# Kernel optimization log

Hardware: AMD Instinct MI355X
Metric: run time of the kernel (lower is better)

Reference implementation:

```python
import jax, jax.numpy as jnp
import numpy as np

EPS = 1e-4
SILU_GAIN = 1.0 / 0.596  # magnitude-preserving SiLU gain
SCALES = (4, 4, 8)       # prod == A_DIM == 128
T = 0.3                  # residual lerp weight


def mp_silu(x):
    return jax.nn.silu(x) * SILU_GAIN


def pixel_norm(x):
    # normalize over channel dim (axis=1) to unit RMS
    return x * jax.lax.rsqrt(jnp.mean(jnp.square(x), axis=1, keepdims=True) + EPS)


def norm_w(w):
    # magnitude-preserving conv: per-output-filter L2-normalized weight
    n = jnp.sqrt(jnp.sum(jnp.square(w), axis=tuple(range(1, w.ndim)), keepdims=True) + 1e-8)
    return w / n


def mp_add(a, b, t=T):
    return (a * (1.0 - t) + b * t) / np.sqrt((1.0 - t) ** 2 + t ** 2)


def conv2d(x, w, groups=1, padding=((0, 0), (0, 0))):
    return jax.lax.conv_general_dilated(
        x, w, (1, 1), padding,
        dimension_numbers=('NCHW', 'OIHW', 'NCHW'), feature_group_count=groups)


def conv1d(x, w, groups=1, padding=((0, 0),)):
    return jax.lax.conv_general_dilated(
        x, w, (1,), padding,
        dimension_numbers=('NCH', 'OIH', 'NCH'), feature_group_count=groups)


def avgpool_freq(x, s):
    B, C, F, L = x.shape
    return jnp.mean(x.reshape(B, C, F // s, s, L), axis=3)


def min_gru(h, w):
    # minGRU: z_t = sigmoid(Wz h_t), c_t = Wc h_t, s_t = (1-z_t) s_{t-1} + z_t c_t
    z, c = jnp.split(conv1d(h, norm_w(w)), 2, axis=1)
    z = jax.nn.sigmoid(z)
    a, b = 1.0 - z, z * c  # linear recurrence s_t = a_t s_{t-1} + b_t

    def comb(x, y):
        a1, b1 = x
        a2, b2 = y
        return a2 * a1, a2 * b1 + b2

    _, out = jax.lax.associative_scan(comb, (a, b), axis=-1)
    return out


def conv_block(x, w1, wd, w2, wdn, s):
    # x: [B, d, F, L]
    x = pixel_norm(x)
    r = mp_silu(x)
    r = conv2d(r, norm_w(w1))                                            # d -> h, 1x1
    r = conv2d(r, norm_w(wd), groups=wd.shape[0], padding=((2, 2), (1, 1)))  # depthwise 5x3
    r = mp_silu(r)
    r = conv2d(r, norm_w(w2))                                            # h -> d, 1x1
    h = mp_add(x, r)
    return conv2d(avgpool_freq(h, s), norm_w(wdn))                       # d -> 2d, freq /s


def seq_block(x, hg_w, dw_w, gru_w, out_w):
    # x: [B, d, L]
    x = pixel_norm(x)
    h, g = jnp.split(conv1d(x, norm_w(hg_w)), 2, axis=1)  # each [B, H, L]
    h = mp_silu(h)
    h = conv1d(h, norm_w(dw_w), groups=dw_w.shape[0], padding=((1, 1),))  # depthwise k=3
    h = mp_silu(h)
    h = min_gru(h, gru_w)
    h = h * mp_silu(g)
    return mp_add(x, conv1d(h, norm_w(out_w)))


def setup_inputs() -> dict:
    key = jax.random.key(0)
    ks = jax.random.split(key, 18)
    rn = lambda k, s: jax.random.normal(k, s, dtype=jnp.float32)
    B, L, A = 2, 2048, 128
    return {
        'audio': rn(ks[0], (B, A, L)),
        'proj_w': rn(ks[1], (64, 1, 1, 1)) * 0.5,
        'proj_b': jnp.zeros((64,), jnp.float32),
        'c0_w1': rn(ks[2], (128, 64, 1, 1)),
        'c0_wd': rn(ks[3], (128, 1, 5, 3)),
        'c0_w2': rn(ks[4], (64, 128, 1, 1)),
        'c0_dn': rn(ks[5], (128, 64, 1, 1)),
        'c1_w1': rn(ks[6], (256, 128, 1, 1)),
        'c1_wd': rn(ks[7], (256, 1, 5, 3)),
        'c1_w2': rn(ks[8], (128, 256, 1, 1)),
        'c1_dn': rn(ks[9], (256, 128, 1, 1)),
        'c2_w1': rn(ks[10], (512, 256, 1, 1)),
        'c2_wd': rn(ks[11], (512, 1, 5, 3)),
        'c2_w2': rn(ks[12], (256, 512, 1, 1)),
        'c2_dn': rn(ks[13], (512, 256, 1, 1)),
        'hg_w': rn(ks[14], (4, 2048, 512, 1)),
        'dw_w': rn(ks[15], (4, 1024, 1, 3)),
        'gru_w': rn(ks[16], (4, 2048, 1024, 1)),
        'out_w': rn(ks[17], (4, 512, 1024, 1)),
    }


def reference(audio, proj_w, proj_b,
              c0_w1, c0_wd, c0_w2, c0_dn,
              c1_w1, c1_wd, c1_w2, c1_dn,
              c2_w1, c2_wd, c2_w2, c2_dn,
              hg_w, dw_w, gru_w, out_w):
    h = audio[:, None]  # [B, 1, A_DIM, L]
    h = conv2d(h, proj_w) + proj_b[None, :, None, None]
    blocks = ((c0_w1, c0_wd, c0_w2, c0_dn),
              (c1_w1, c1_wd, c1_w2, c1_dn),
              (c2_w1, c2_wd, c2_w2, c2_dn))
    for (w1, wd, w2, dn), s in zip(blocks, SCALES):
        h = conv_block(h, w1, wd, w2, dn, s)
    h = h[:, :, 0, :]  # freq dim reduced to 1 -> [B, dim, L]
    for i in range(hg_w.shape[0]):
        h = seq_block(h, hg_w[i], dw_w[i], gru_w[i], out_w[i])
    return mp_silu(h)
```

## Files before the change

### kernel.cpp

```cpp
#include <hip/hip_runtime.h>
#include <math.h>

#define GAIN 1.6778523489932886f
#define MPS  1.3130643285972254f

typedef __attribute__((ext_vector_type(8))) short short8;
typedef __attribute__((ext_vector_type(4))) short short4v;
typedef __attribute__((ext_vector_type(4))) float float4v;

__device__ __forceinline__ float silu_g(float x){
  float s = 1.0f/(1.0f + __expf(-x));
  return x*s*GAIN;
}
__device__ __forceinline__ short f2bf(float f){
  unsigned u = __builtin_bit_cast(unsigned, f);
  u += 0x7fffu + ((u >> 16) & 1u);
  return (short)(u >> 16);
}
__device__ __forceinline__ float bf2f(unsigned short h){
  return __builtin_bit_cast(float, ((unsigned)h) << 16);
}

typedef __attribute__((address_space(3))) unsigned int as3_uint;
typedef const __attribute__((address_space(1))) unsigned int as1_cuint;
__device__ __forceinline__ void gload16(const unsigned short* gsrc, unsigned short* ldst){
  __builtin_amdgcn_global_load_lds((as1_cuint*)gsrc, (as3_uint*)ldst, 16, 0, 0);
}

struct NcEnt { const float* w; int O, K, dstOff; };
struct NcArgs { NcEnt e[16]; };

__global__ __launch_bounds__(64) void normcast_kernel(NcArgs na, unsigned short* __restrict__ wbf){
  int row = blockIdx.x;
  int base = 0; int i;
  for (i = 0; i < 16; i++){
    if (row < base + na.e[i].O) break;
    base += na.e[i].O;
  }
  if (i >= 16) return;
  int r = row - base; int K = na.e[i].K;
  const float* w = na.e[i].w + (long)r*K;
  unsigned short* dst = wbf + na.e[i].dstOff + (long)r*K;
  int tid = threadIdx.x;
  float s = 0.f;
  const bool v4 = ((K & 3) == 0);
  if (v4){
    for (int k = tid*4; k < K; k += 256){
      float4v v = *(const float4v*)&w[k];
      s += v[0]*v[0] + v[1]*v[1] + v[2]*v[2] + v[3]*v[3];
    }
  } else {
    for (int k = tid; k < K; k += 64){ float v = w[k]; s += v*v; }
  }
  for (int off = 32; off; off >>= 1) s += __shfl_down(s, off);
  float inv = rsqrtf(__shfl(s, 0) + 1e-8f);
  if (v4){
    for (int k = tid*4; k < K; k += 256){
      float4v v = *(const float4v*)&w[k];
      short4v o = { f2bf(v[0]*inv), f2bf(v[1]*inv), f2bf(v[2]*inv), f2bf(v[3]*inv) };
      *(short4v*)&dst[k] = o;
    }
  } else {
    for (int k = tid; k < K; k += 64) dst[k] = (unsigned short)f2bf(w[k]*inv);
  }
}

__global__ __launch_bounds__(64) void projstats_kernel(const float* __restrict__ pw, const float* __restrict__ pb,
                                                       float* __restrict__ S){
  int t = threadIdx.x;
  float p = pw[t], q = pb[t];
  float s1 = p*p, s2 = p*q, s3 = q*q;
  for (int off = 32; off; off >>= 1){
    s1 += __shfl_down(s1, off); s2 += __shfl_down(s2, off); s3 += __shfl_down(s3, off);
  }
  if (t == 0){ S[0] = s1; S[1] = s2; S[2] = s3; }
}

__global__ __launch_bounds__(256) void invn_audio_kernel(const float* __restrict__ audio, const float* __restrict__ S,
                                                         float* __restrict__ invn){
  long i = blockIdx.x*256 + threadIdx.x;
  if (i >= (2L*128*2048)/4) return;
  long e = i*4;
  float S1 = S[0], S2 = S[1], S3 = S[2];
  float4v a = *(const float4v*)&audio[e];
  float4v o;
  #pragma unroll
  for (int j = 0; j < 4; j++) o[j] = rsqrtf((a[j]*a[j]*S1 + 2.f*a[j]*S2 + S3)/64.f + 1e-4f);
  *(float4v*)&invn[e] = o;
}

template<int G, bool BF>
__global__ __launch_bounds__(256) void invn_reduce_kernel(const void* __restrict__ Xv, float* __restrict__ invn,
                                                          int C, int F){
  constexpr int L = 256/G;
  int t = threadIdx.x; int cs = t / L; int li = t % L;
  long pos = (long)blockIdx.x*L + li;
  int bf = (int)(pos >> 11); int l = (int)(pos & 2047);
  int b = bf / F; int f = bf - b*F;
  long base = ((long)b*C*F + f)*2048 + l;
  long stride = (long)F*2048;
  float s = 0.f;
  if (BF){
    const unsigned short* X = (const unsigned short*)Xv;
    for (int c = cs; c < C; c += G){ float v = bf2f(X[base + (long)c*stride]); s += v*v; }
  } else {
    const float* X = (const float*)Xv;
    for (int c = cs; c < C; c += G){ float v = X[base + (long)c*stride]; s += v*v; }
  }
  __shared__ float red[256];
  red[t] = s; __syncthreads();
  #pragma unroll
  for (int off = G/2; off > 0; off >>= 1){
    if (cs < off) red[t] += red[t + off*L];
    __syncthreads();
  }
  if (cs == 0) invn[pos] = rsqrtf(red[li]/(float)C + 1e-4f);
}

__global__ __launch_bounds__(256) void normT_kernel(const float* __restrict__ SEQ,
                                                    const float* __restrict__ invn,
                                                    unsigned short* __restrict__ XST){
  __shared__ float tile[64][65];
  const int l0 = blockIdx.x*64, c0 = blockIdx.y*64, b = blockIdx.z;
  const int t = threadIdx.x;
  const int lr = (t & 15)*4;
  const int cr = t >> 4;
  #pragma unroll
  for (int p = 0; p < 4; p++){
    int c = cr + p*16;
    float4v v = *(const float4v*)&SEQ[((long)(b*512 + c0 + c))*2048 + l0 + lr];
    tile[c][lr+0] = v[0]; tile[c][lr+1] = v[1]; tile[c][lr+2] = v[2]; tile[c][lr+3] = v[3];
  }
  __syncthreads();
  const int cc = (t & 7)*8;
  const int lw = t >> 3;
  #pragma unroll
  for (int p = 0; p < 2; p++){
    int l = lw + p*32;
    float iv = invn[b*2048 + l0 + l];
    short8 o;
    #pragma unroll
    for (int j = 0; j < 8; j++) o[j] = f2bf(tile[cc+j][l] * iv);
    *(short8*)&XST[((long)(b*2048 + l0 + l))*512 + c0 + cc] = o;
  }
}

struct GTArgs {
  const unsigned short* A;
  const unsigned short* B;
  unsigned short* O1;
  unsigned short* O2;
  int N, K;
};

template<int EMODE>
__global__ __launch_bounds__(256,2) void gemmT_kernel(GTArgs g){
  __shared__ __align__(16) char SMEMraw[49152];
  unsigned short (*Asm)[4096] = (unsigned short (*)[4096])SMEMraw;
  unsigned short (*Bsm)[4096] = (unsigned short (*)[4096])(SMEMraw + 24576);
  const int t = threadIdx.x;
  const int lane = t & 63;
  const int wc = (t >> 7) & 1;
  const int wsd = (t >> 6) & 1;
  const int q = lane >> 4, r16 = lane & 15;
  const int m0 = blockIdx.x * 128;
  const int n0 = blockIdx.y * 128;
  const int K = g.K;

  const int r0 = t >> 2;
  const int c8 = (((t & 3) ^ ((r0 >> 1) & 3)) << 3);
  const unsigned short* Ap = g.A + (long)(n0 + r0)*K + c8;
  const unsigned short* Bp = g.B + (long)(m0 + r0)*K + c8;

  auto stage = [&](int bi, int k0){
    gload16(Ap + k0,           &Asm[bi][t*8]);
    gload16(Ap + 64*K + k0,    &Asm[bi][2048 + t*8]);
    gload16(Bp + k0,           &Bsm[bi][t*8]);
    gload16(Bp + 64*K + k0,    &Bsm[bi][2048 + t*8]);
  };

  float4v acc[4][4];
  #pragma unroll
  for (int i = 0; i < 4; i++)
    #pragma unroll
    for (int j = 0; j < 4; j++) acc[i][j] = (float4v){0.f,0.f,0.f,0.f};

  const int nit = K >> 5;
  stage(0, 0);
  stage(1, 32);

  const int qsw = ((q ^ ((r16 >> 1) & 3)) << 3);

  for (int it = 0; it < nit; ++it){
    if (it + 2 < nit){
      stage((it + 2) % 3, (it + 2) << 5);
      asm volatile("" ::: "memory");
      asm volatile("s_waitcnt vmcnt(8)" ::: "memory");
    } else if (it + 1 < nit){
      asm volatile("s_waitcnt vmcnt(4)" ::: "memory");
    } else {
      asm volatile("s_waitcnt vmcnt(0)" ::: "memory");
    }
    __builtin_amdgcn_s_barrier();
    asm volatile("" ::: "memory");

    const unsigned short* As = Asm[it % 3];
    const unsigned short* Bs = Bsm[it % 3];
    short8 afr[4], bfr[4];
    #pragma unroll
    for (int i = 0; i < 4; i++) afr[i] = *(const short8*)&As[(wc*64 + i*16 + r16)*32 + qsw];
    #pragma unroll
    for (int j = 0; j < 4; j++) bfr[j] = *(const short8*)&Bs[(wsd*64 + j*16 + r16)*32 + qsw];
    #pragma unroll
    for (int i = 0; i < 4; i++)
      #pragma unroll
      for (int j = 0; j < 4; j++)
        acc[i][j] = __builtin_amdgcn_mfma_f32_16x16x32_bf16(afr[i], bfr[j], acc[i][j], 0, 0, 0);

    asm volatile("" ::: "memory");
    __builtin_amdgcn_s_barrier();
  }

  if (EMODE == 1 && n0 < 1024){
    float* Cf = (float*)SMEMraw;
    #pragma unroll
    for (int h = 0; h < 2; h++){
      __syncthreads();
      if (wc == h){
        #pragma unroll
        for (int j = 0; j < 4; j++){
          int m = wsd*64 + j*16 + r16;
          #pragma unroll
          for (int i = 0; i < 4; i++)
            *(float4v*)&Cf[m*68 + i*16 + q*4] = acc[i][j];
        }
      }
      __syncthreads();
      #pragma unroll
      for (int p = 0; p < 4; p++){
        int m = (t >> 3) + p*32;
        int n8 = (t & 7)*8;
        int gm = m0 + m; int b = gm >> 11, l = gm & 2047;
        float4v v0 = *(const float4v*)&Cf[m*68 + n8];
        float4v v1 = *(const float4v*)&Cf[m*68 + n8 + 4];
        short8 o;
        #pragma unroll
        for (int e = 0; e < 4; e++){ o[e] = f2bf(silu_g(v0[e])); o[e+4] = f2bf(silu_g(v1[e])); }
        *(short8*)&g.O1[((long)(b*2048 + l))*1024 + (n0 + h*64 + n8)] = o;
      }
    }
  } else {
    float* Csm = (float*)SMEMraw;
    #pragma unroll
    for (int qtr = 0; qtr < 4; qtr++){
      __syncthreads();
      if (wc == (qtr >> 1)){
        #pragma unroll
        for (int ii = 0; ii < 2; ii++){
          int i = (qtr & 1)*2 + ii;
          #pragma unroll
          for (int j = 0; j < 4; j++){
            int m = wsd*64 + j*16 + r16;
            #pragma unroll
            for (int rg = 0; rg < 4; rg++)
              Csm[(ii*16 + q*4 + rg)*132 + m] = acc[i][j][rg];
          }
        }
      }
      __syncthreads();
      #pragma unroll
      for (int sp = 0; sp < 2; sp++){
        int nrow = (t >> 4) + sp*16;
        int n = n0 + qtr*32 + nrow;
        int m8 = (t & 15)*8;
        int gm = m0 + m8; int b = gm >> 11, l = gm & 2047;
        float4v v0 = *(const float4v*)&Csm[nrow*132 + m8];
        float4v v1 = *(const float4v*)&Csm[nrow*132 + m8 + 4];
        short8 o;
        #pragma unroll
        for (int e = 0; e < 4; e++){ o[e] = f2bf(v0[e]); o[e+4] = f2bf(v1[e]); }
        if (EMODE == 1) *(short8*)&g.O2[((long)(b*1024 + (n - 1024)))*2048 + l] = o;
        else            *(short8*)&g.O1[((long)(b*2048 + n))*2048 + l] = o;
      }
    }
  }
}

struct GemmArgs {
  const unsigned short* A;
  const unsigned short* Bh;
  const float* invn; const float* audio;
  const float* pw; const float* pb;
  const unsigned short* auxXH;
  unsigned short* CoutH; unsigned short* Cout2H;
  int N, K, Fdim, Lw, lq0, BLw, Bl0, CLw, Cl0, Nsto, Fsrc;
};

template<int BMODE, int EMODE>
__global__ __launch_bounds__(256,2) void mgemm_kernel(GemmArgs g){
  __shared__ __align__(16) char SMEMraw[20480];
  unsigned short* Asm = (unsigned short*)SMEMraw;
  unsigned short* Bsm = Asm + 128*40;
  const int t = threadIdx.x;
  const int lane = t & 63;
  const int wave = t >> 6;
  const int wc = wave >> 1, wsd = wave & 1;
  const int q = lane >> 4, r16 = lane & 15;
  const int s0 = blockIdx.x * 128;
  const int n0 = blockIdx.y * 128;
  const int FL = g.Fdim * g.Lw;

  const int ar = t >> 1, ah = t & 1;
  const int an = n0 + ar;
  const bool aval = an < g.N;
  const unsigned short* Aptr = g.A + (long)an*g.K + ah*16;

  const int kg = t & 7, mg = t >> 3;
  const int mb = s0 + mg*4;
  int bcol = mb / FL; int rr = mb - bcol*FL;
  int fcol = (g.Fdim > 1) ? (rr / g.Lw) : 0;
  int labs = g.lq0 + (rr - fcol*g.Lw);
  const bool cv = (bcol < 2);
  bool lv[4];
  #pragma unroll
  for (int j = 0; j < 4; j++) lv[j] = cv && (labs + j >= 0) && (labs + j < 2048);
  const bool vec4 = cv && (labs >= 0) && (labs + 3 < 2048);
  const unsigned short* bbase = g.Bh;
  if (cv) bbase = g.Bh + ((long)(bcol*g.K)*g.Fsrc + fcol)*g.BLw + (labs - g.Bl0);
  const long kstep = (long)g.Fsrc * g.BLw;

  float invn4[4] = {0,0,0,0}, aud4[4] = {0,0,0,0};
  if (BMODE == 2 || BMODE == 3){
    #pragma unroll
    for (int j = 0; j < 4; j++) if (lv[j]){
      invn4[j] = g.invn[(bcol*g.Fdim + fcol)*2048 + labs + j];
      if (BMODE == 2) aud4[j] = g.audio[(bcol*128 + fcol)*2048 + labs + j];
    }
  }

  float4v acc[4][4];
  #pragma unroll
  for (int i = 0; i < 4; i++)
    #pragma unroll
    for (int j = 0; j < 4; j++) acc[i][j] = (float4v){0.f,0.f,0.f,0.f};

  short8 pa0 = {0,0,0,0,0,0,0,0}, pa1 = {0,0,0,0,0,0,0,0};
  short4v praw[4];
  #pragma unroll
  for (int i = 0; i < 4; i++) praw[i] = (short4v){0,0,0,0};

  auto ldA = [&](int kb){
    if (aval){
      pa0 = *(const short8*)(Aptr + kb);
      pa1 = *(const short8*)(Aptr + kb + 8);
    }
  };
  auto ldB = [&](int kb){
    #pragma unroll
    for (int i = 0; i < 4; i++){
      const int k = kb + kg*4 + i;
      const unsigned short* bp = bbase + (long)k*kstep;
      if (vec4) praw[i] = *(const short4v*)bp;
      else {
        short4v u = {0,0,0,0};
        #pragma unroll
        for (int j = 0; j < 4; j++) if (lv[j]) u[j] = (short)bp[j];
        praw[i] = u;
      }
    }
  };

  ldA(0);
  if (BMODE != 2) ldB(0);

  for (int k0 = 0; k0 < g.K; k0 += 32){
    short8 sa0 = pa0, sa1 = pa1;
    short4v bpk[4];
    if (BMODE == 0){
      #pragma unroll
      for (int j = 0; j < 4; j++){
        short4v p;
        #pragma unroll
        for (int i = 0; i < 4; i++) p[i] = praw[i][j];
        bpk[j] = p;
      }
    } else if (BMODE == 3){
      #pragma unroll
      for (int j = 0; j < 4; j++){
        short4v p;
        #pragma unroll
        for (int i = 0; i < 4; i++)
          p[i] = f2bf(silu_g(bf2f((unsigned short)praw[i][j]) * invn4[j]));
        bpk[j] = p;
      }
    } else {
      float tv[4][4];
      #pragma unroll
      for (int i = 0; i < 4; i++){
        const int k = k0 + kg*4 + i;
        const float pwk = g.pw[k], pbk = g.pb[k];
        #pragma unroll
        for (int j = 0; j < 4; j++) tv[i][j] = lv[j] ? silu_g((aud4[j]*pwk + pbk)*invn4[j]) : 0.f;
      }
      #pragma unroll
      for (int j = 0; j < 4; j++){
        short4v p;
        #pragma unroll
        for (int i = 0; i < 4; i++) p[i] = f2bf(tv[i][j]);
        bpk[j] = p;
      }
    }
    if (k0 + 32 < g.K){
      ldA(k0 + 32);
      if (BMODE != 2) ldB(k0 + 32);
    }

    __syncthreads();
    *(short8*)&Asm[ar*40 + ah*16]     = sa0;
    *(short8*)&Asm[ar*40 + ah*16 + 8] = sa1;
    #pragma unroll
    for (int j = 0; j < 4; j++)
      *(short4v*)&Bsm[(mg*4 + j)*40 + kg*4] = bpk[j];
    __syncthreads();

    short8 afr[4], bfr[4];
    #pragma unroll
    for (int i = 0; i < 4; i++) afr[i] = *(const short8*)&Asm[(wc*64 + i*16 + r16)*40 + q*8];
    #pragma unroll
    for (int j = 0; j < 4; j++) bfr[j] = *(const short8*)&Bsm[(wsd*64 + j*16 + r16)*40 + q*8];
    #pragma unroll
    for (int i = 0; i < 4; i++)
      #pragma unroll
      for (int j = 0; j < 4; j++)
        acc[i][j] = __builtin_amdgcn_mfma_f32_16x16x32_bf16(afr[i], bfr[j], acc[i][j], 0, 0, 0);
  }

  {
    float* Csm = (float*)SMEMraw;
    #pragma unroll
    for (int qtr = 0; qtr < 4; qtr++){
      __syncthreads();
      if (wc == (qtr >> 1)){
        #pragma unroll
        for (int ii = 0; ii < 2; ii++){
          int i = (qtr & 1)*2 + ii;
          #pragma unroll
          for (int j = 0; j < 4; j++){
            int m = wsd*64 + j*16 + r16;
            #pragma unroll
            for (int rg = 0; rg < 4; rg++)
              Csm[(ii*16 + q*4 + rg)*132 + m] = acc[i][j][rg];
          }
        }
      }
      __syncthreads();
      #pragma unroll
      for (int sp = 0; sp < 2; sp++){
        int nrow = (t >> 4) + sp*16;
        int n = n0 + qtr*32 + nrow;
        int m8 = (t & 15)*8;
        if (n >= g.N) continue;
        int sg = s0 + m8;
        int b2 = sg / FL; int r2 = sg - b2*FL;
        if (b2 >= 2) continue;
        int f2 = (g.Fdim > 1) ? (r2 / g.Lw) : 0;
        int l2 = g.lq0 + (r2 - f2*g.Lw);
        float4v v0 = *(const float4v*)&Csm[nrow*132 + m8];
        float4v v1 = *(const float4v*)&Csm[nrow*132 + m8 + 4];
        long obase = ((long)(b2*g.Nsto + n)*g.Fdim + f2)*g.CLw + (l2 - g.Cl0);
        short8 o;
        if (EMODE == 1){
          #pragma unroll
          for (int e = 0; e < 4; e++){ o[e] = f2bf(v0[e]); o[e+4] = f2bf(v1[e]); }
        } else if (EMODE == 2){
          short8 axv = *(const short8*)&g.auxXH[((long)(b2*g.N + n)*g.Fdim + f2)*2048 + l2];
          const float* ivp = &g.invn[(b2*g.Fdim + f2)*2048 + l2];
          float4v iv0 = *(const float4v*)ivp;
          float4v iv1 = *(const float4v*)(ivp + 4);
          #pragma unroll
          for (int e = 0; e < 4; e++){
            float xn0 = bf2f((unsigned short)axv[e]) * iv0[e];
            float xn1 = bf2f((unsigned short)axv[e+4]) * iv1[e];
            o[e]   = f2bf((xn0*0.7f + v0[e]*0.3f)*MPS);
            o[e+4] = f2bf((xn1*0.7f + v1[e]*0.3f)*MPS);
          }
        } else {
          float pwn = g.pw[n], pbn = g.pb[n];
          const float* ap  = &g.audio[(b2*128 + f2)*2048 + l2];
          const float* ivp = &g.invn[(b2*g.Fdim + f2)*2048 + l2];
          float4v a0 = *(const float4v*)ap,  a1 = *(const float4v*)(ap + 4);
          float4v iv0 = *(const float4v*)ivp, iv1 = *(const float4v*)(ivp + 4);
          #pragma unroll
          for (int e = 0; e < 4; e++){
            float xn0 = (a0[e]*pwn + pbn)*iv0[e];
            float xn1 = (a1[e]*pwn + pbn)*iv1[e];
            o[e]   = f2bf((xn0*0.7f + v0[e]*0.3f)*MPS);
            o[e+4] = f2bf((xn1*0.7f + v1[e]*0.3f)*MPS);
          }
        }
        *(short8*)&g.CoutH[obase] = o;
      }
    }
  }
}

struct DnArgs {
  const unsigned short* A; const unsigned short* P;
  float* Cout; unsigned short* CoutH;
  int N, K, F2, Lc, l0;
};

template<int EMODE>
__global__ __launch_bounds__(256,4) void mgemm64_kernel(DnArgs g){
  __shared__ __align__(16) char SMEM[10240];
  unsigned short* Asm = (unsigned short*)SMEM;
  unsigned short* Bsm = Asm + 64*40;
  const int t = threadIdx.x;
  const int lane = t & 63;
  const int wave = t >> 6;
  const int wc = wave >> 1, wsd = wave & 1;
  const int q = lane >> 4, r16 = lane & 15;
  const int s0 = blockIdx.x * 64;
  const int n0 = blockIdx.y * 64;
  const int FL = g.F2 * g.Lc;

  const int ar = t >> 2, ah = t & 3;
  const unsigned short* Aptr = g.A + (long)(n0 + ar)*g.K + ah*8;
  const int kg = t & 7, mg = t >> 3;
  const bool bstage = (mg < 16);
  const int mb = s0 + (mg & 15)*4;
  const int bcol = mb / FL; const int rr = mb - bcol*FL;
  const int fcol = rr / g.Lc; const int li = rr - fcol*g.Lc;
  const unsigned short* bbase = g.P + ((long)(bcol*g.K)*g.F2 + fcol)*g.Lc + li;
  const long kstep = (long)g.F2 * g.Lc;

  float4v acc[2][2];
  #pragma unroll
  for (int i = 0; i < 2; i++)
    #pragma unroll
    for (int j = 0; j < 2; j++) acc[i][j] = (float4v){0.f,0.f,0.f,0.f};

  short8 pa = {0,0,0,0,0,0,0,0};
  short4v praw[4];
  #pragma unroll
  for (int i = 0; i < 4; i++) praw[i] = (short4v){0,0,0,0};

  auto ldA = [&](int kb){ pa = *(const short8*)(Aptr + kb); };
  auto ldB = [&](int kb){
    if (bstage){
      #pragma unroll
      for (int i = 0; i < 4; i++)
        praw[i] = *(const short4v*)(bbase + (long)(kb + kg*4 + i)*kstep);
    }
  };
  ldA(0); ldB(0);

  for (int k0 = 0; k0 < g.K; k0 += 32){
    short8 sa = pa;
    short4v bpk[4];
    #pragma unroll
    for (int j = 0; j < 4; j++){
      short4v p;
      #pragma unroll
      for (int i = 0; i < 4; i++) p[i] = praw[i][j];
      bpk[j] = p;
    }
    if (k0 + 32 < g.K){ ldA(k0 + 32); ldB(k0 + 32); }

    __syncthreads();
    *(short8*)&Asm[ar*40 + ah*8] = sa;
    if (bstage){
      #pragma unroll
      for (int j = 0; j < 4; j++)
        *(short4v*)&Bsm[((mg & 15)*4 + j)*40 + kg*4] = bpk[j];
    }
    __syncthreads();

    short8 afr[2], bfr[2];
    #pragma unroll
    for (int i = 0; i < 2; i++) afr[i] = *(const short8*)&Asm[(wc*32 + i*16 + r16)*40 + q*8];
    #pragma unroll
    for (int j = 0; j < 2; j++) bfr[j] = *(const short8*)&Bsm[(wsd*32 + j*16 + r16)*40 + q*8];
    #pragma unroll
    for (int i = 0; i < 2; i++)
      #pragma unroll
      for (int j = 0; j < 2; j++)
        acc[i][j] = __builtin_amdgcn_mfma_f32_16x16x32_bf16(afr[i], bfr[j], acc[i][j], 0, 0, 0);
  }

  {
    float* Csm = (float*)SMEM;
    const int b2 = s0 / FL; const int r20 = s0 - b2*FL;
    const int f2c = r20 / g.Lc; const int l2c = g.l0 + (r20 - f2c*g.Lc);
    #pragma unroll
    for (int nq = 0; nq < 4; nq++){
      __syncthreads();
      if (wc == (nq >> 1)){
        const int i = nq & 1;
        #pragma unroll
        for (int j = 0; j < 2; j++)
          #pragma unroll
          for (int rg = 0; rg < 4; rg++)
            Csm[(q*4 + rg)*68 + wsd*32 + j*16 + r16] = acc[i][j][rg];
      }
      __syncthreads();
      int nrow = t >> 4;
      int mq = (t & 15)*4;
      int n = n0 + nq*16 + nrow;
      float4v v = *(const float4v*)&Csm[nrow*68 + mq];
      long oidx = ((long)(b2*g.N + n)*g.F2 + f2c)*2048 + l2c + mq;
      if (EMODE == 0){
        *(float4v*)&g.Cout[oidx] = v;
      } else {
        short4v o = { f2bf(v[0]), f2bf(v[1]), f2bf(v[2]), f2bf(v[3]) };
        *(short4v*)&g.CoutH[oidx] = o;
      }
    }
  }
}

template<int EMODE>
__global__ __launch_bounds__(256,4) void seqout_kernel(const unsigned short* __restrict__ A,
                                                       const unsigned short* __restrict__ Bh,
                                                       const float* __restrict__ invn,
                                                       const float* __restrict__ auxX,
                                                       float* __restrict__ Cout, int K){
  __shared__ __align__(16) char SMEM[10240];
  unsigned short* Asm = (unsigned short*)SMEM;
  unsigned short* Bsm = Asm + 64*40;
  const int t = threadIdx.x;
  const int lane = t & 63;
  const int wave = t >> 6;
  const int wc = wave >> 1, wsd = wave & 1;
  const int q = lane >> 4, r16 = lane & 15;
  const int s0 = blockIdx.x * 64;
  const int n0 = blockIdx.y * 64;

  const int ar = t >> 2, ah = t & 3;
  const unsigned short* Aptr = A + (long)(n0 + ar)*K + ah*8;
  const int kg = t & 7, mg = t >> 3;
  const bool bstage = (mg < 16);
  const int mb = s0 + (mg & 15)*4;
  const int bcol = mb >> 11, lb = mb & 2047;
  const unsigned short* bbase = Bh + ((long)bcol*K)*2048 + lb;

  float4v acc[2][2];
  #pragma unroll
  for (int i = 0; i < 2; i++)
    #pragma unroll
    for (int j = 0; j < 2; j++) acc[i][j] = (float4v){0.f,0.f,0.f,0.f};

  short8 pa = {0,0,0,0,0,0,0,0};
  short4v praw[4];
  #pragma unroll
  for (int i = 0; i < 4; i++) praw[i] = (short4v){0,0,0,0};

  auto ldA = [&](int kb){ pa = *(const short8*)(Aptr + kb); };
  auto ldB = [&](int kb){
    if (bstage){
      #pragma unroll
      for (int i = 0; i < 4; i++)
        praw[i] = *(const short4v*)(bbase + (long)(kb + kg*4 + i)*2048);
    }
  };
  ldA(0); ldB(0);

  for (int k0 = 0; k0 < K; k0 += 32){
    short8 sa = pa;
    short4v bpk[4];
    #pragma unroll
    for (int j = 0; j < 4; j++){
      short4v p;
      #pragma unroll
      for (int i = 0; i < 4; i++) p[i] = praw[i][j];
      bpk[j] = p;
    }
    if (k0 + 32 < K){ ldA(k0 + 32); ldB(k0 + 32); }

    __syncthreads();
    *(short8*)&Asm[ar*40 + ah*8] = sa;
    if (bstage){
      #pragma unroll
      for (int j = 0; j < 4; j++)
        *(short4v*)&Bsm[((mg & 15)*4 + j)*40 + kg*4] = bpk[j];
    }
    __syncthreads();

    short8 afr[2], bfr[2];
    #pragma unroll
    for (int i = 0; i < 2; i++) afr[i] = *(const short8*)&Asm[(wc*32 + i*16 + r16)*40 + q*8];
    #pragma unroll
    for (int j = 0; j < 2; j++) bfr[j] = *(const short8*)&Bsm[(wsd*32 + j*16 + r16)*40 + q*8];
    #pragma unroll
    for (int i = 0; i < 2; i++)
      #pragma unroll
      for (int j = 0; j < 2; j++)
        acc[i][j] = __builtin_amdgcn_mfma_f32_16x16x32_bf16(afr[i], bfr[j], acc[i][j], 0, 0, 0);
  }

  {
    float* Csm = (float*)SMEM;
    const int b2 = s0 >> 11; const int l0b = s0 & 2047;
    #pragma unroll
    for (int nq = 0; nq < 4; nq++){
      __syncthreads();
      if (wc == (nq >> 1)){
        const int i = nq & 1;
        #pragma unroll
        for (int j = 0; j < 2; j++)
          #pragma unroll
          for (int rg = 0; rg < 4; rg++)
            Csm[(q*4 + rg)*68 + wsd*32 + j*16 + r16] = acc[i][j][rg];
      }
      __syncthreads();
      int nrow = t >> 4;
      int mq = (t & 15)*4;
      int n = n0 + nq*16 + nrow;
      int l = l0b + mq;
      float4v v = *(const float4v*)&Csm[nrow*68 + mq];
      float4v ax = *(const float4v*)&auxX[((long)b2*512 + n)*2048 + l];
      float4v iv = *(const float4v*)&invn[b2*2048 + l];
      float4v r;
      #pragma unroll
      for (int e = 0; e < 4; e++){
        float xn = ax[e]*iv[e];
        float rr = (xn*0.7f + v[e]*0.3f)*MPS;
        r[e] = (EMODE == 6) ? silu_g(rr) : rr;
      }
      *(float4v*)&Cout[((long)b2*512 + n)*2048 + l] = r;
    }
  }
}

__global__ __launch_bounds__(256) void poolf_kernel(const unsigned short* __restrict__ Hb,
                                                    unsigned short* __restrict__ P,
                                                    int F2, int s, int Lc, long total4){
  long i = blockIdx.x*256 + threadIdx.x;
  if (i >= total4) return;
  long e = i*4;
  int li = (int)(e % Lc); long r0 = e / Lc;
  int f2 = (int)(r0 % F2); long r = r0 / F2;
  const unsigned short* src = Hb + ((long)r*F2*s + (long)f2*s)*Lc + li;
  float a0=0,a1=0,a2=0,a3=0;
  for (int p = 0; p < s; p++){
    short4v u = *(const short4v*)(src + (long)p*Lc);
    a0 += bf2f((unsigned short)u[0]); a1 += bf2f((unsigned short)u[1]);
    a2 += bf2f((unsigned short)u[2]); a3 += bf2f((unsigned short)u[3]);
  }
  float inv = 1.f/(float)s;
  short4v o = { f2bf(a0*inv), f2bf(a1*inv), f2bf(a2*inv), f2bf(a3*inv) };
  *(short4v*)&P[((long)r*F2 + f2)*Lc + li] = o;
}

struct DwArgs { const unsigned short* R1; const unsigned short* wd; unsigned short* R2; int C, F, Lc, l0; };
__global__ __launch_bounds__(256) void dw2d_kernel(DwArgs a){
  int idx = blockIdx.x*256 + threadIdx.x;
  int Lq = a.Lc >> 3;
  int Fq = a.F >> 2;
  int total = 2*a.C*Fq*Lq;
  if (idx >= total) return;
  int lq = idx % Lq; int r = idx / Lq;
  int fq = r % Fq; r /= Fq;
  int c = r % a.C; int b = r / a.C;
  int f0 = fq*4;
  int labs = a.l0 + lq*8;
  int Lw = a.Lc + 8;
  const unsigned short* base = a.R1 + (long)((b*a.C + c)*a.F)*Lw + (labs - (a.l0 - 4));
  const unsigned short* w = a.wd + c*15;
  float W[5][3];
  #pragma unroll
  for (int tp = 0; tp < 5; tp++)
    #pragma unroll
    for (int j = 0; j < 3; j++) W[tp][j] = bf2f(w[tp*3 + j]);

  const bool llo = (labs > 0);
  const bool lhi = (labs + 8 < 2048);
  float acc[4][8];
  #pragma unroll
  for (int t = 0; t < 4; t++)
    #pragma unroll
    for (int j = 0; j < 8; j++) acc[t][j] = 0.f;

  #pragma unroll
  for (int r8 = 0; r8 < 8; r8++){
    int rrow = f0 - 2 + r8;
    if (rrow < 0 || rrow >= a.F) continue;
    const unsigned short* p = base + (long)rrow*Lw;
    short4v u0 = *(const short4v*)p;
    short4v u1 = *(const short4v*)(p + 4);
    float x[10];
    x[0] = llo ? bf2f(p[-1]) : 0.f;
    x[1] = bf2f((unsigned short)u0[0]); x[2] = bf2f((unsigned short)u0[1]);
    x[3] = bf2f((unsigned short)u0[2]); x[4] = bf2f((unsigned short)u0[3]);
    x[5] = bf2f((unsigned short)u1[0]); x[6] = bf2f((unsigned short)u1[1]);
    x[7] = bf2f((unsigned short)u1[2]); x[8] = bf2f((unsigned short)u1[3]);
    x[9] = lhi ? bf2f(p[8]) : 0.f;
    #pragma unroll
    for (int t = 0; t < 4; t++){
      const int df = r8 - 2 - t;
      if (df < -2 || df > 2) continue;
      float w0 = W[df+2][0], w1 = W[df+2][1], w2 = W[df+2][2];
      #pragma unroll
      for (int j = 0; j < 8; j++)
        acc[t][j] += w0*x[j] + w1*x[j+1] + w2*x[j+2];
    }
  }

  unsigned short* ob = a.R2 + ((long)((b*a.C + c)*a.F + f0))*a.Lc + (labs - a.l0);
  #pragma unroll
  for (int t = 0; t < 4; t++){
    short8 o;
    #pragma unroll
    for (int j = 0; j < 8; j++) o[j] = f2bf(silu_g(acc[t][j]));
    *(short8*)(ob + (long)t*a.Lc) = o;
  }
}

__global__ __launch_bounds__(256) void dwseqT_kernel(const unsigned short* __restrict__ HST,
                                                     const unsigned short* __restrict__ w,
                                                     unsigned short* __restrict__ H2T){
  int idx = blockIdx.x*256 + threadIdx.x;
  if (idx >= 2*2048*128) return;
  int c0 = (idx & 127) * 8; long bt = idx >> 7;
  int tt = (int)(bt & 2047);
  const unsigned short* base = HST + bt*1024 + c0;
  short8 zz = {0,0,0,0,0,0,0,0};
  short8 x1 = *(const short8*)base;
  short8 x0 = (tt > 0)    ? *(const short8*)(base - 1024) : zz;
  short8 x2 = (tt < 2047) ? *(const short8*)(base + 1024) : zz;
  const unsigned short* wp = w + c0*3;
  short8 o;
  #pragma unroll
  for (int j = 0; j < 8; j++){
    float w0 = bf2f(wp[3*j]), w1 = bf2f(wp[3*j+1]), w2 = bf2f(wp[3*j+2]);
    float v = w0*bf2f((unsigned short)x0[j]) + w1*bf2f((unsigned short)x1[j]) + w2*bf2f((unsigned short)x2[j]);
    o[j] = f2bf(silu_g(v));
  }
  *(short8*)&H2T[bt*1024 + c0] = o;
}

__global__ __launch_bounds__(256) void scan_kernel(const unsigned short* __restrict__ ZC, const unsigned short* __restrict__ G,
                                                   unsigned short* __restrict__ SC){
  int bc = blockIdx.x;
  int b = bc >> 10, c = bc & 1023;
  const unsigned short* zrow = ZC + ((long)(b*2048 + c))*2048;
  const unsigned short* crow = ZC + ((long)(b*2048 + 1024 + c))*2048;
  const unsigned short* grow = G + (long)bc*2048;
  unsigned short* orow = SC + (long)bc*2048;
  int tid = threadIdx.x;
  int t0 = tid*8;
  short8 zv = *(const short8*)&zrow[t0];
  short8 cv = *(const short8*)&crow[t0];
  float av[8], bv[8];
  float A = 1.f, Bv = 0.f;
  #pragma unroll
  for (int j = 0; j < 8; j++){
    float z = bf2f((unsigned short)zv[j]); float cval = bf2f((unsigned short)cv[j]);
    float zs = 1.f/(1.f + __expf(-z));
    float a = 1.f - zs; float bb = zs*cval;
    av[j] = a; bv[j] = bb;
    Bv = a*Bv + bb;
    A = a*A;
  }
  __shared__ float sA[256], sB[256];
  sA[tid] = A; sB[tid] = Bv;
  __syncthreads();
  for (int off = 1; off < 256; off <<= 1){
    float pA = 1.f, pB = 0.f;
    if (tid >= off){ pA = sA[tid-off]; pB = sB[tid-off]; }
    __syncthreads();
    float nA = A*pA; float nB = A*pB + Bv;
    A = nA; Bv = nB;
    sA[tid] = A; sB[tid] = Bv;
    __syncthreads();
  }
  float h = (tid > 0) ? sB[tid-1] : 0.f;
  short8 gv = *(const short8*)&grow[t0];
  short8 ov;
  #pragma unroll
  for (int j = 0; j < 8; j++){
    h = av[j]*h + bv[j];
    ov[j] = f2bf(h * silu_g(bf2f((unsigned short)gv[j])));
  }
  *(short8*)&orow[t0] = ov;
}

extern "C" void kernel_launch(void* const* d_in, const int* in_sizes, int n_in,
                              void* d_out, int out_size, void* d_ws, size_t ws_size,
                              hipStream_t stream) {
  const float* audio = (const float*)d_in[0];
  const float* pw = (const float*)d_in[1];
  const float* pb = (const float*)d_in[2];
  const float* cw1[3] = {(const float*)d_in[3], (const float*)d_in[7], (const float*)d_in[11]};
  const float* cwd[3] = {(const float*)d_in[4], (const float*)d_in[8], (const float*)d_in[12]};
  const float* cw2[3] = {(const float*)d_in[5], (const float*)d_in[9], (const float*)d_in[13]};
  const float* cdn[3] = {(const float*)d_in[6], (const float*)d_in[10], (const float*)d_in[14]};
  const float* hgw  = (const float*)d_in[15];
  const float* dww  = (const float*)d_in[16];
  const float* gruw = (const float*)d_in[17];
  const float* outw = (const float*)d_in[18];
  float* out = (float*)d_out;

  char* P0 = (char*)d_ws;
  float*          INVW = (float*)P0;                    P0 += 131072;
  unsigned short* WBF  = (unsigned short*)P0;           P0 += 30443776;
  float*          INVN = (float*)P0;                    P0 += 2097152;
  char*           XBZC = P0;                            P0 += 33554432;
  unsigned short* IN1h = (unsigned short*)P0;           P0 += 33554432;
  unsigned short* IN2h = (unsigned short*)P0;           P0 += 16777216;
  float*          SEQ  = (float*)P0;                    P0 += 8388608;
  char*           ARENA = P0;
  long arenaBytes = (long)ws_size - (long)(P0 - (char*)d_ws);
  float* S = INVW + 32000;

  const float* wsrc[16] = {cw1[0],cwd[0],cw2[0],cdn[0], cw1[1],cwd[1],cw2[1],cdn[1],
                           cw1[2],cwd[2],cw2[2],cdn[2], hgw, dww, gruw, outw};
  int Os[16] = {128,128,64,128, 256,256,128,256, 512,512,256,512, 8192,4096,8192,2048};
  int Ks[16] = {64,15,128,64, 128,15,256,128, 256,15,512,256, 512,3,1024,1024};
  int wbfOff[16];
  {
    int wo = 0;
    for (int i = 0; i < 16; i++){ wbfOff[i] = wo; wo += Os[i]*Ks[i]; }
  }
  {
    NcArgs na;
    int rows = 0;
    for (int i = 0; i < 16; i++){
      na.e[i].w = wsrc[i]; na.e[i].O = Os[i]; na.e[i].K = Ks[i]; na.e[i].dstOff = wbfOff[i];
      rows += Os[i];
    }
    normcast_kernel<<<rows, 64, 0, stream>>>(na, WBF);
  }
  projstats_kernel<<<1, 64, 0, stream>>>(pw, pb, S);

  int Cin_[3]  = {64,128,256};
  int Cmid_[3] = {128,256,512};
  int F_[3]    = {128,32,8};
  int s_[3]    = {4,4,8};
  const unsigned short* XinH[3] = {nullptr, IN1h, IN2h};
  unsigned short* XoutH[3] = {IN1h, IN2h, nullptr};
  int iW1[3]={0,4,8}, iWd[3]={1,5,9}, iW2[3]={2,6,10}, iDn[3]={3,7,11};

  for (int b = 0; b < 3; b++){
    int Cin = Cin_[b], Cmid = Cmid_[b], F = F_[b], s = s_[b];
    int F2 = F/s;
    int nc = 16;
    for (int c = 1; c <= 16; c <<= 1){
      long Lc = 2048/c;
      long bytes = 2L*(2L*Cmid*F*(Lc+8) + 2L*Cmid*F*Lc + 2L*Cin*F*Lc + 2L*Cin*F2*Lc);
      if (bytes <= arenaBytes){ nc = c; break; }
    }
    int Lc = 2048/nc;
    unsigned short* R1 = (unsigned short*)ARENA;
    unsigned short* R2 = R1 + 2L*Cmid*F*(Lc+8);
    unsigned short* Hb = R2 + 2L*Cmid*F*Lc;
    unsigned short* Pb = Hb + 2L*Cin*F*Lc;

    if (b == 0){
      invn_audio_kernel<<<(2*128*2048/4+255)/256, 256, 0, stream>>>(audio, S, INVN);
    } else {
      int positions = 2*F*2048;
      invn_reduce_kernel<8,true><<<positions/32, 256, 0, stream>>>(XinH[b], INVN, Cin, F);
    }

    for (int ci = 0; ci < nc; ci++){
      int l0 = ci*Lc;
      GemmArgs ga{};
      ga.A = WBF + wbfOff[iW1[b]];
      ga.Bh = XinH[b]; ga.invn = INVN; ga.audio = audio; ga.pw = pw; ga.pb = pb;
      ga.CoutH = R1; ga.N = Cmid; ga.K = Cin; ga.Fdim = F; ga.Lw = Lc+8; ga.lq0 = l0-4;
      ga.BLw = 2048; ga.Bl0 = 0; ga.CLw = Lc+8; ga.Cl0 = l0-4; ga.Nsto = Cmid; ga.Fsrc = F;
      int M1 = 2*F*(Lc+8);
      dim3 g1((M1+127)/128, (Cmid+127)/128);
      if (b == 0) mgemm_kernel<2,1><<<g1,256,0,stream>>>(ga);
      else        mgemm_kernel<3,1><<<g1,256,0,stream>>>(ga);
      DwArgs da{R1, WBF + wbfOff[iWd[b]], R2, Cmid, F, Lc, l0};
      int tdw = 2*Cmid*(F/4)*(Lc/8);
      dw2d_kernel<<<(tdw+255)/256, 256, 0, stream>>>(da);
      GemmArgs gb{};
      gb.A = WBF + wbfOff[iW2[b]];
      gb.Bh = R2; gb.invn = INVN; gb.audio = audio; gb.pw = pw; gb.pb = pb; gb.auxXH = XinH[b];
      gb.CoutH = Hb; gb.N = Cin; gb.K = Cmid; gb.Fdim = F; gb.Lw = Lc; gb.lq0 = l0;
      gb.BLw = Lc; gb.Bl0 = l0; gb.CLw = Lc; gb.Cl0 = l0; gb.Nsto = Cin; gb.Fsrc = F;
      int M2 = 2*F*Lc;
      dim3 g2((M2+127)/128, (Cin+127)/128);
      if (b == 0) mgemm_kernel<0,3><<<g2,256,0,stream>>>(gb);
      else        mgemm_kernel<0,2><<<g2,256,0,stream>>>(gb);
      long tp4 = (2L*Cin*F2*Lc)/4;
      poolf_kernel<<<(int)((tp4+255)/256), 256, 0, stream>>>(Hb, Pb, F2, s, Lc, tp4);
      DnArgs dn{};
      dn.A = WBF + wbfOff[iDn[b]]; dn.P = Pb;
      dn.Cout = SEQ; dn.CoutH = XoutH[b];
      dn.N = Cmid; dn.K = Cin; dn.F2 = F2; dn.Lc = Lc; dn.l0 = l0;
      dim3 gdn((2*F2*Lc)/64, Cmid/64);
      if (b == 2) mgemm64_kernel<0><<<gdn,256,0,stream>>>(dn);
      else        mgemm64_kernel<1><<<gdn,256,0,stream>>>(dn);
    }
  }

  unsigned short* XST = IN1h;
  unsigned short* HST = XST + 2097152;
  unsigned short* G   = HST + 4194304;
  unsigned short* H2T = G  + 4194304;
  unsigned short* SC  = H2T + 4194304;
  unsigned short* ZCh = (unsigned short*)XBZC;

  for (int i = 0; i < 4; i++){
    invn_reduce_kernel<16,false><<<4096/16, 256, 0, stream>>>(SEQ, INVN, 512, 1);
    normT_kernel<<<dim3(32,8,2), 256, 0, stream>>>(SEQ, INVN, XST);
    GTArgs gh{ WBF + wbfOff[12] + (long)i*2048*512, XST, HST, G, 2048, 512 };
    gemmT_kernel<1><<<dim3(32,16), 256, 0, stream>>>(gh);
    dwseqT_kernel<<<2048, 256, 0, stream>>>(HST, WBF + wbfOff[13] + i*1024*3, H2T);
    GTArgs gz{ WBF + wbfOff[14] + (long)i*2048*1024, H2T, ZCh, nullptr, 2048, 1024 };
    gemmT_kernel<0><<<dim3(32,16), 256, 0, stream>>>(gz);
    scan_kernel<<<2048,256,0,stream>>>(ZCh, G, SC);
    const unsigned short* oA = WBF + wbfOff[15] + (long)i*512*1024;
    if (i < 3) seqout_kernel<5><<<dim3(64,8),256,0,stream>>>(oA, SC, INVN, SEQ, SEQ, 1024);
    else       seqout_kernel<6><<<dim3(64,8),256,0,stream>>>(oA, SC, INVN, SEQ, out, 1024);
  }

  (void)in_sizes; (void)n_in; (void)out_size;
}
```

Before: 1.108 ms.

## Precompute normalized SiLU input once and widen depthwise conv frequency tile

For conv blocks 1 and 2, a new elementwise kernel applies pixel-norm scaling and SiLU to the block input once, writing a bf16 buffer. The first 1x1 GEMM then reads that buffer as a plain operand instead of recomputing the norm and SiLU inside every GEMM tile. Separately, the depthwise 5x3 kernel now computes 8 frequency rows per thread instead of 4, so more outputs share each loaded row. The trade-off is an extra full read and write of the activation tensor, plus higher register pressure in the depthwise kernel.

```diff
diff --git a/kernel.cpp b/kernel.cpp
--- a/kernel.cpp
+++ b/kernel.cpp
@@ -117,6 +117,32 @@
   if (cs == 0) invn[pos] = rsqrtf(red[li]/(float)C + 1e-4f);
 }
 
+template<bool SILU, bool BF>
+__global__ __launch_bounds__(256) void applynorm_kernel(const void* __restrict__ Xv, const float* __restrict__ invn,
+                                                        unsigned short* __restrict__ XB, int C, int F, long total4){
+  long i = blockIdx.x*256 + threadIdx.x;
+  if (i >= total4) return;
+  long e = i*4;
+  int l = (int)(e & 2047); long r = e >> 11;
+  int f = (int)(r % F); long bc = r / F; int b = (int)(bc / C);
+  float4v x;
+  if (BF){
+    short4v u = *(const short4v*)((const unsigned short*)Xv + e);
+    x = (float4v){ bf2f((unsigned short)u[0]), bf2f((unsigned short)u[1]),
+                   bf2f((unsigned short)u[2]), bf2f((unsigned short)u[3]) };
+  } else {
+    x = *(const float4v*)((const float*)Xv + e);
+  }
+  float4v iv = *(const float4v*)&invn[((long)b*F + f)*2048 + l];
+  short4v o;
+  #pragma unroll
+  for (int j = 0; j < 4; j++){
+    float v = x[j]*iv[j];
+    o[j] = f2bf(SILU ? silu_g(v) : v);
+  }
+  *(short4v*)&XB[e] = o;
+}
+
 __global__ __launch_bounds__(256) void normT_kernel(const float* __restrict__ SEQ,
                                                     const float* __restrict__ invn,
                                                     unsigned short* __restrict__ XST){
@@ -330,11 +356,11 @@
   const long kstep = (long)g.Fsrc * g.BLw;
 
   float invn4[4] = {0,0,0,0}, aud4[4] = {0,0,0,0};
-  if (BMODE == 2 || BMODE == 3){
+  if (BMODE == 2){
     #pragma unroll
     for (int j = 0; j < 4; j++) if (lv[j]){
       invn4[j] = g.invn[(bcol*g.Fdim + fcol)*2048 + labs + j];
-      if (BMODE == 2) aud4[j] = g.audio[(bcol*128 + fcol)*2048 + labs + j];
+      aud4[j]  = g.audio[(bcol*128 + fcol)*2048 + labs + j];
     }
   }
 
@@ -371,7 +397,7 @@
   };
 
   ldA(0);
-  if (BMODE != 2) ldB(0);
+  if (BMODE == 0) ldB(0);
 
   for (int k0 = 0; k0 < g.K; k0 += 32){
     short8 sa0 = pa0, sa1 = pa1;
@@ -384,15 +410,6 @@
         for (int i = 0; i < 4; i++) p[i] = praw[i][j];
         bpk[j] = p;
       }
-    } else if (BMODE == 3){
-      #pragma unroll
-      for (int j = 0; j < 4; j++){
-        short4v p;
-        #pragma unroll
-        for (int i = 0; i < 4; i++)
-          p[i] = f2bf(silu_g(bf2f((unsigned short)praw[i][j]) * invn4[j]));
-        bpk[j] = p;
-      }
     } else {
       float tv[4][4];
       #pragma unroll
@@ -412,7 +429,7 @@
     }
     if (k0 + 32 < g.K){
       ldA(k0 + 32);
-      if (BMODE != 2) ldB(k0 + 32);
+      if (BMODE == 0) ldB(k0 + 32);
     }
 
     __syncthreads();
@@ -756,13 +773,13 @@
 __global__ __launch_bounds__(256) void dw2d_kernel(DwArgs a){
   int idx = blockIdx.x*256 + threadIdx.x;
   int Lq = a.Lc >> 3;
-  int Fq = a.F >> 2;
+  int Fq = a.F >> 3;
   int total = 2*a.C*Fq*Lq;
   if (idx >= total) return;
   int lq = idx % Lq; int r = idx / Lq;
   int fq = r % Fq; r /= Fq;
   int c = r % a.C; int b = r / a.C;
-  int f0 = fq*4;
+  int f0 = fq*8;
   int labs = a.l0 + lq*8;
   int Lw = a.Lc + 8;
   const unsigned short* base = a.R1 + (long)((b*a.C + c)*a.F)*Lw + (labs - (a.l0 - 4));
@@ -775,15 +792,15 @@
 
   const bool llo = (labs > 0);
   const bool lhi = (labs + 8 < 2048);
-  float acc[4][8];
-  #pragma unroll
-  for (int t = 0; t < 4; t++)
+  float acc[8][8];
+  #pragma unroll
+  for (int t = 0; t < 8; t++)
     #pragma unroll
     for (int j = 0; j < 8; j++) acc[t][j] = 0.f;
 
   #pragma unroll
-  for (int r8 = 0; r8 < 8; r8++){
-    int rrow = f0 - 2 + r8;
+  for (int r12 = 0; r12 < 12; r12++){
+    int rrow = f0 - 2 + r12;
     if (rrow < 0 || rrow >= a.F) continue;
     const unsigned short* p = base + (long)rrow*Lw;
     short4v u0 = *(const short4v*)p;
@@ -796,8 +813,8 @@
     x[7] = bf2f((unsigned short)u1[2]); x[8] = bf2f((unsigned short)u1[3]);
     x[9] = lhi ? bf2f(p[8]) : 0.f;
     #pragma unroll
-    for (int t = 0; t < 4; t++){
-      const int df = r8 - 2 - t;
+    for (int t = 0; t < 8; t++){
+      const int df = r12 - 2 - t;
       if (df < -2 || df > 2) continue;
       float w0 = W[df+2][0], w1 = W[df+2][1], w2 = W[df+2][2];
       #pragma unroll
@@ -808,7 +825,7 @@
 
   unsigned short* ob = a.R2 + ((long)((b*a.C + c)*a.F + f0))*a.Lc + (labs - a.l0);
   #pragma unroll
-  for (int t = 0; t < 4; t++){
+  for (int t = 0; t < 8; t++){
     short8 o;
     #pragma unroll
     for (int j = 0; j < 8; j++) o[j] = f2bf(silu_g(acc[t][j]));
@@ -955,27 +972,30 @@
     unsigned short* R2 = R1 + 2L*Cmid*F*(Lc+8);
     unsigned short* Hb = R2 + 2L*Cmid*F*Lc;
     unsigned short* Pb = Hb + 2L*Cin*F*Lc;
+    unsigned short* XB = (unsigned short*)XBZC;
 
     if (b == 0){
       invn_audio_kernel<<<(2*128*2048/4+255)/256, 256, 0, stream>>>(audio, S, INVN);
     } else {
       int positions = 2*F*2048;
       invn_reduce_kernel<8,true><<<positions/32, 256, 0, stream>>>(XinH[b], INVN, Cin, F);
+      long total4 = (long)2*Cin*F*2048/4;
+      applynorm_kernel<true,true><<<(int)((total4+255)/256), 256, 0, stream>>>(XinH[b], INVN, XB, Cin, F, total4);
     }
 
     for (int ci = 0; ci < nc; ci++){
       int l0 = ci*Lc;
       GemmArgs ga{};
       ga.A = WBF + wbfOff[iW1[b]];
-      ga.Bh = XinH[b]; ga.invn = INVN; ga.audio = audio; ga.pw = pw; ga.pb = pb;
+      ga.Bh = XB; ga.invn = INVN; ga.audio = audio; ga.pw = pw; ga.pb = pb;
       ga.CoutH = R1; ga.N = Cmid; ga.K = Cin; ga.Fdim = F; ga.Lw = Lc+8; ga.lq0 = l0-4;
       ga.BLw = 2048; ga.Bl0 = 0; ga.CLw = Lc+8; ga.Cl0 = l0-4; ga.Nsto = Cmid; ga.Fsrc = F;
       int M1 = 2*F*(Lc+8);
       dim3 g1((M1+127)/128, (Cmid+127)/128);
       if (b == 0) mgemm_kernel<2,1><<<g1,256,0,stream>>>(ga);
-      else        mgemm_kernel<3,1><<<g1,256,0,stream>>>(ga);
+      else        mgemm_kernel<0,1><<<g1,256,0,stream>>>(ga);
       DwArgs da{R1, WBF + wbfOff[iWd[b]], R2, Cmid, F, Lc, l0};
-      int tdw = 2*Cmid*(F/4)*(Lc/8);
+      int tdw = 2*Cmid*(F/8)*(Lc/8);
       dw2d_kernel<<<(tdw+255)/256, 256, 0, stream>>>(da);
       GemmArgs gb{};
       gb.A = WBF + wbfOff[iW2[b]];
```

After: 1.216 ms. 1.1x slower.
